# Performance work log

Measured on AMD Instinct MI355X. Metric: run time of the kernel, lower is better.

## Reference

```python
import jax, jax.numpy as jnp
import numpy as np

HIDDEN = 768
NUM_HEADS = 12
HEAD_DIM = HIDDEN // NUM_HEADS
QMAX = 127.0
DOMAIN_MIN, DOMAIN_MAX = -10.0, 0.0
NUM_INTERVALS = 12


def _build_pla_coeffs():
    # Least-squares linear fit of exp(x) on each of 12 uniform intervals of [-10, 0].
    xs = np.linspace(DOMAIN_MIN, DOMAIN_MAX, 1001)
    ys = np.exp(xs)
    edges = np.linspace(DOMAIN_MIN, DOMAIN_MAX, NUM_INTERVALS + 1)
    ms, cs = [], []
    for i in range(NUM_INTERVALS):
        mask = (xs >= edges[i]) & (xs <= edges[i + 1])
        m, c = np.polyfit(xs[mask], ys[mask], 1)
        ms.append(m)
        cs.append(c)
    # 'intervals' buffer holds the left endpoints a_i (length 12), as in torch code
    return (np.asarray(ms, np.float32), np.asarray(cs, np.float32),
            edges[:NUM_INTERVALS].astype(np.float32))

_PLA_M, _PLA_C, _PLA_A = _build_pla_coeffs()


def pla_exp(x):
    m = jnp.asarray(_PLA_M)
    c = jnp.asarray(_PLA_C)
    a = jnp.asarray(_PLA_A)
    xc = jnp.clip(x, DOMAIN_MIN, DOMAIN_MAX)
    # sum(xc >= a_i) - 1 == searchsorted(a, xc, side='right') - 1 (a is sorted)
    idx = jnp.clip(jnp.searchsorted(a, xc, side='right') - 1, 0, NUM_INTERVALS - 2)
    return m[idx] * xc + c[idx]


def pla_softmax(scores):
    shifted = scores - jnp.max(scores, axis=-1, keepdims=True)
    exps = pla_exp(shifted)
    return exps / (jnp.sum(exps, axis=-1, keepdims=True) + 1e-9)


def quant_linear(x, w_int8, w_scale, bias):
    # Dynamic per-token symmetric int8 quantization of activations.
    abs_max = jnp.max(jnp.abs(x), axis=-1, keepdims=True)
    input_scale = abs_max / QMAX
    input_scale = jnp.where(input_scale == 0.0, 1.0, input_scale)
    x_q = jnp.clip(jnp.round(x / input_scale), -128.0, 127.0)  # int8 values in fp32
    out = x_q @ w_int8.astype(jnp.float32).T                   # simulated int32 accum
    out = out * w_scale * input_scale                          # dequant rescale
    return out + bias


def setup_inputs() -> dict:
    key = jax.random.key(0)
    ks = jax.random.split(key, 16)
    B, S = 4, 1024
    inp = {
        'hidden_states': jax.random.normal(ks[0], (B, S, HIDDEN), jnp.float32),
        'attention_mask': jnp.zeros((B, 1, 1, S), jnp.float32),
    }
    for i, name in enumerate(['q', 'k', 'v', 'o']):
        kw, ksc, kb = ks[1 + 3 * i], ks[2 + 3 * i], ks[3 + 3 * i]
        inp[f'w{name}_int8'] = jax.random.randint(kw, (HIDDEN, HIDDEN), 0, 256, jnp.int32) - 128
        inp[f'w{name}_scale'] = jax.random.uniform(ksc, (HIDDEN,), jnp.float32) * 1e-4
        inp[f'b{name}'] = jax.random.normal(kb, (HIDDEN,), jnp.float32)
    return inp


def reference(hidden_states, attention_mask,
              wq_int8, wq_scale, bq,
              wk_int8, wk_scale, bk,
              wv_int8, wv_scale, bv,
              wo_int8, wo_scale, bo):
    B, S, H = hidden_states.shape
    scale = HEAD_DIM ** -0.5

    def split_heads(x):  # [B,S,H] -> [B,nh,S,hd]
        return x.reshape(B, S, NUM_HEADS, HEAD_DIM).transpose(0, 2, 1, 3)

    q = split_heads(quant_linear(hidden_states, wq_int8, wq_scale, bq))
    k = split_heads(quant_linear(hidden_states, wk_int8, wk_scale, bk))
    v = split_heads(quant_linear(hidden_states, wv_int8, wv_scale, bv))

    attn_scores = jnp.einsum('bhqd,bhkd->bhqk', q, k) * scale
    attn_scores = attn_scores + attention_mask
    attn_probs = pla_softmax(attn_scores)  # dropout is identity in eval mode

    context = jnp.einsum('bhqk,bhkd->bhqd', attn_probs, v)
    context = context.transpose(0, 2, 1, 3).reshape(B, S, H)
    return quant_linear(context, wo_int8, wo_scale, bo)
```

## Files before the change

kernel.cpp:

```cpp
#include <hip/hip_runtime.h>
#include <stdint.h>
#include <cmath>

#define TOKENS 4096
#define HIDDEN 768
#define NHEADS 12
#define SEQ    1024
#define NBH    48

typedef int   int32x4 __attribute__((ext_vector_type(4)));
typedef float f32x4   __attribute__((ext_vector_type(4)));
typedef short short8  __attribute__((ext_vector_type(8)));

struct PlaCoeffs { float m[12]; float c[12]; };

#define WBYTES   ((size_t)HIDDEN * HIDDEN)
#define OFF_WQ    ((size_t)256)
#define OFF_WK    (OFF_WQ + WBYTES)
#define OFF_WV    (OFF_WK + WBYTES)
#define OFF_WO    (OFF_WV + WBYTES)
#define OFF_XQ1   (OFF_WO + WBYTES)
#define OFF_SC1   (OFF_XQ1 + (size_t)TOKENS * HIDDEN)
#define OFF_QH    (OFF_SC1 + (size_t)TOKENS * 4)
#define HB        ((size_t)NBH * SEQ * 64 * 2)
#define OFF_KH    (OFF_QH + HB)
#define OFF_VT    (OFF_KH + HB)
#define OFF_CTX   (OFF_VT + HB)
#define OFF_XQ2   (OFF_CTX + (size_t)TOKENS * HIDDEN * 4)
#define OFF_SC2   (OFF_XQ2 + (size_t)TOKENS * HIDDEN)

__device__ __forceinline__ unsigned short f2bf(float f) {
  unsigned int u = __float_as_uint(f);
  u = (u + 0x7fffu + ((u >> 16) & 1u)) >> 16;
  return (unsigned short)u;
}

__device__ __forceinline__ unsigned int cvtpk_bf16(float a, float b) {
  unsigned int r;
  asm volatile("v_cvt_pk_bf16_f32 %0, %1, %2" : "=v"(r) : "v"(a), "v"(b));
  return r;
}

static PlaCoeffs compute_pla_coeffs() {
  PlaCoeffs out;
  const double step_e = 10.0 / 12.0;
  for (int i = 0; i < 12; i++) {
    double e0 = (double)i * step_e + (-10.0);
    double e1 = (i + 1 == 12) ? 0.0 : (double)(i + 1) * step_e + (-10.0);
    double n = 0.0, Sx = 0.0, Sy = 0.0, Sxy = 0.0, Sxx = 0.0;
    for (int j = 0; j <= 1000; j++) {
      double x = (j == 1000) ? 0.0 : (double)j * 0.01 + (-10.0);
      if (x >= e0 && x <= e1) {
        double y = std::exp(x);
        n += 1.0; Sx += x; Sy += y; Sxy += x * y; Sxx += x * x;
      }
    }
    double det = n * Sxx - Sx * Sx;
    double m = (n * Sxy - Sx * Sy) / det;
    double c = (Sy - m * Sx) / n;
    out.m[i] = (float)m;
    out.c[i] = (float)c;
  }
  return out;
}
static const PlaCoeffs g_pla = compute_pla_coeffs();

__global__ void prep_kernel(const float* __restrict__ x, signed char* __restrict__ xq,
                            float* __restrict__ sc,
                            const int* __restrict__ w0, const int* __restrict__ w1,
                            const int* __restrict__ w2, const int* __restrict__ w3,
                            signed char* __restrict__ o0, signed char* __restrict__ o1,
                            signed char* __restrict__ o2, signed char* __restrict__ o3) {
  int tid = threadIdx.x;
  if (blockIdx.x < TOKENS) {
    int t = blockIdx.x;
    const float* row = x + (size_t)t * HIDDEN;
    float v0 = row[tid], v1 = row[tid + 256], v2 = row[tid + 512];
    float am = fmaxf(fabsf(v0), fmaxf(fabsf(v1), fabsf(v2)));
#pragma unroll
    for (int m = 1; m < 64; m <<= 1) am = fmaxf(am, __shfl_xor(am, m, 64));
    __shared__ float red[4];
    if ((tid & 63) == 0) red[tid >> 6] = am;
    __syncthreads();
    float total = fmaxf(fmaxf(red[0], red[1]), fmaxf(red[2], red[3]));
    float s = total / 127.0f;
    if (s == 0.0f) s = 1.0f;
    float q0 = fminf(fmaxf(rintf(v0 / s), -128.0f), 127.0f);
    float q1 = fminf(fmaxf(rintf(v1 / s), -128.0f), 127.0f);
    float q2 = fminf(fmaxf(rintf(v2 / s), -128.0f), 127.0f);
    signed char* orow = xq + (size_t)t * HIDDEN;
    orow[tid]       = (signed char)(int)q0;
    orow[tid + 256] = (signed char)(int)q1;
    orow[tid + 512] = (signed char)(int)q2;
    if (tid == 0) sc[t] = s;
  } else {
    int p = blockIdx.x - TOKENS;
    int z = p / 576, px = p % 576;
    const int* src = z == 0 ? w0 : z == 1 ? w1 : z == 2 ? w2 : w3;
    signed char* dst = z == 0 ? o0 : z == 1 ? o1 : z == 2 ? o2 : o3;
    int idx = (px * 256 + tid) * 4;
    int32x4 v = *(const int32x4*)(src + idx);
    int packed = (v[0] & 255) | ((v[1] & 255) << 8) | ((v[2] & 255) << 16) | (v[3] << 24);
    *(int*)(dst + idx) = packed;
  }
}

__global__ void quant_kernel(const float* __restrict__ x, signed char* __restrict__ xq,
                             float* __restrict__ sc) {
  int t = blockIdx.x;
  int tid = threadIdx.x;
  const float* row = x + (size_t)t * HIDDEN;
  float v0 = row[tid], v1 = row[tid + 256], v2 = row[tid + 512];
  float am = fmaxf(fabsf(v0), fmaxf(fabsf(v1), fabsf(v2)));
#pragma unroll
  for (int m = 1; m < 64; m <<= 1) am = fmaxf(am, __shfl_xor(am, m, 64));
  __shared__ float red[4];
  if ((tid & 63) == 0) red[tid >> 6] = am;
  __syncthreads();
  float total = fmaxf(fmaxf(red[0], red[1]), fmaxf(red[2], red[3]));
  float s = total / 127.0f;
  if (s == 0.0f) s = 1.0f;
  float q0 = fminf(fmaxf(rintf(v0 / s), -128.0f), 127.0f);
  float q1 = fminf(fmaxf(rintf(v1 / s), -128.0f), 127.0f);
  float q2 = fminf(fmaxf(rintf(v2 / s), -128.0f), 127.0f);
  signed char* orow = xq + (size_t)t * HIDDEN;
  orow[tid]       = (signed char)(int)q0;
  orow[tid + 256] = (signed char)(int)q1;
  orow[tid + 512] = (signed char)(int)q2;
  if (tid == 0) sc[t] = s;
}

__device__ __forceinline__ void i8_mainloop(const signed char* __restrict__ Abase,
                                            const signed char* __restrict__ Bbase,
                                            char* As, char* Bs, int tid,
                                            int32x4 acc[4][4]) {
  int lane = tid & 63, w = tid >> 6;
  int lr = lane & 15, lg = lane >> 4;
  int wr = w >> 1, wc = w & 1;
  int laneoff = (lane >> 3) * HIDDEN + (((lane & 7) ^ (lane >> 3)) * 16);
  int rowblk = w * 32;

#pragma unroll
  for (int ii = 0; ii < 4; ii++) {
    const signed char* sa = Abase + (size_t)(rowblk + ii * 8) * HIDDEN + laneoff;
    const signed char* sb = Bbase + (size_t)(rowblk + ii * 8) * HIDDEN + laneoff;
    __builtin_amdgcn_global_load_lds(
        (const __attribute__((address_space(1))) void*)sa,
        (__attribute__((address_space(3))) void*)(As + (w * 4 + ii) * 1024), 16, 0, 0);
    __builtin_amdgcn_global_load_lds(
        (const __attribute__((address_space(1))) void*)sb,
        (__attribute__((address_space(3))) void*)(Bs + (w * 4 + ii) * 1024), 16, 0, 0);
  }
  __syncthreads();

  int buf = 0;
  for (int ks = 0; ks < 6; ks++) {
    if (ks < 5) {
      char* An = As + (buf ^ 1) * 16384;
      char* Bn = Bs + (buf ^ 1) * 16384;
#pragma unroll
      for (int ii = 0; ii < 4; ii++) {
        const signed char* sa =
            Abase + (size_t)(rowblk + ii * 8) * HIDDEN + (ks + 1) * 128 + laneoff;
        const signed char* sb =
            Bbase + (size_t)(rowblk + ii * 8) * HIDDEN + (ks + 1) * 128 + laneoff;
        __builtin_amdgcn_global_load_lds(
            (const __attribute__((address_space(1))) void*)sa,
            (__attribute__((address_space(3))) void*)(An + (w * 4 + ii) * 1024), 16, 0, 0);
        __builtin_amdgcn_global_load_lds(
            (const __attribute__((address_space(1))) void*)sb,
            (__attribute__((address_space(3))) void*)(Bn + (w * 4 + ii) * 1024), 16, 0, 0);
      }
    }
    const char* Ac = As + buf * 16384;
    const char* Bc = Bs + buf * 16384;
#pragma unroll
    for (int ksub = 0; ksub < 2; ksub++) {
      int32x4 af[4], bf[4];
      int cs = (ksub * 4 + lg) ^ (lr & 7);
#pragma unroll
      for (int i = 0; i < 4; i++)
        af[i] = *(const int32x4*)(Ac + (wr * 64 + i * 16 + lr) * 128 + cs * 16);
#pragma unroll
      for (int j = 0; j < 4; j++)
        bf[j] = *(const int32x4*)(Bc + (wc * 64 + j * 16 + lr) * 128 + cs * 16);
#pragma unroll
      for (int i = 0; i < 4; i++)
#pragma unroll
        for (int j = 0; j < 4; j++)
          acc[i][j] = __builtin_amdgcn_mfma_i32_16x16x64_i8(af[i], bf[j], acc[i][j], 0, 0, 0);
    }
    __syncthreads();
    buf ^= 1;
  }
}

__launch_bounds__(256, 2)
__global__ void qkv_gemm(const signed char* __restrict__ xq, const float* __restrict__ isc,
                         const signed char* __restrict__ wq, const signed char* __restrict__ wk,
                         const signed char* __restrict__ wv,
                         const float* __restrict__ wsq, const float* __restrict__ wsk,
                         const float* __restrict__ wsv,
                         const float* __restrict__ bq, const float* __restrict__ bk,
                         const float* __restrict__ bv,
                         unsigned short* __restrict__ qh, unsigned short* __restrict__ kh,
                         unsigned short* __restrict__ vt) {
  __shared__ __align__(16) char As[2 * 16384];
  __shared__ __align__(16) char Bs[2 * 16384];
  int z = blockIdx.z;
  const signed char* w   = z == 0 ? wq  : z == 1 ? wk  : wv;
  const float*       wsc = z == 0 ? wsq : z == 1 ? wsk : wsv;
  const float*       bias= z == 0 ? bq  : z == 1 ? bk  : bv;
  unsigned short*    out = z == 0 ? qh  : z == 1 ? kh  : vt;

  int tid = threadIdx.x;
  int lane = tid & 63, wave = tid >> 6;
  int lr = lane & 15, lg = lane >> 4;
  int mbase0 = blockIdx.x * 128;
  int mbase = mbase0 + (wave >> 1) * 64;
  int nbase = blockIdx.y * 128 + (wave & 1) * 64;

  int32x4 acc[4][4];
#pragma unroll
  for (int i = 0; i < 4; i++)
#pragma unroll
    for (int j = 0; j < 4; j++) acc[i][j] = (int32x4){0, 0, 0, 0};

  i8_mainloop(xq + (size_t)mbase0 * HIDDEN,
              w + (size_t)blockIdx.y * 128 * HIDDEN, As, Bs, tid, acc);

  if (z < 2) {
#pragma unroll
    for (int j = 0; j < 4; j++) {
      int col = nbase + j * 16 + lr;
      float wsv_ = wsc[col], bv_ = bias[col];
      int h = col >> 6, d = col & 63;
#pragma unroll
      for (int i = 0; i < 4; i++) {
#pragma unroll
        for (int r = 0; r < 4; r++) {
          int trow = mbase + i * 16 + lg * 4 + r;
          float v = (float)acc[i][j][r] * wsv_ * isc[trow] + bv_;
          int bb = trow >> 10, ss = trow & 1023;
          out[(((size_t)(bb * NHEADS + h)) * SEQ + ss) * 64 + d] = f2bf(v);
        }
      }
    }
  } else {
    unsigned short* T = (unsigned short*)As;
#pragma unroll
    for (int j = 0; j < 4; j++) {
      int colc = (wave & 1) * 64 + j * 16 + lr;
      int gcol = blockIdx.y * 128 + colc;
      float wsv_ = wsc[gcol], bv_ = bias[gcol];
      int rlb = (wave >> 1) * 64 + lg * 4;
#pragma unroll
      for (int i = 0; i < 4; i++) {
        int rl = rlb + i * 16;
        float v0 = (float)acc[i][j][0] * wsv_ * isc[mbase0 + rl + 0] + bv_;
        float v1 = (float)acc[i][j][1] * wsv_ * isc[mbase0 + rl + 1] + bv_;
        float v2 = (float)acc[i][j][2] * wsv_ * isc[mbase0 + rl + 2] + bv_;
        float v3 = (float)acc[i][j][3] * wsv_ * isc[mbase0 + rl + 3] + bv_;
        int oct = (rl >> 3) ^ (colc & 7);
        unsigned short* dst = T + colc * 128 + (oct << 3) + (rl & 7);
        *(unsigned int*)(dst)     = cvtpk_bf16(v0, v1);
        *(unsigned int*)(dst + 2) = cvtpk_bf16(v2, v3);
      }
    }
    __syncthreads();
    int bb = mbase0 >> 10, ssb = mbase0 & 1023;
    int o = tid & 15, cb = (tid >> 4) * 8;
#pragma unroll
    for (int j = 0; j < 8; j++) {
      int colc = cb + j;
      int gcol = blockIdx.y * 128 + colc;
      int hh = gcol >> 6, dd = gcol & 63;
      unsigned short* g = out + (((size_t)(bb * NHEADS + hh)) * 64 + dd) * SEQ + ssb + o * 8;
      *(short8*)g = *(const short8*)(T + colc * 128 + ((o ^ (colc & 7)) << 3));
    }
  }
}

__launch_bounds__(256, 2)
__global__ void o_gemm(const signed char* __restrict__ xq, const float* __restrict__ isc,
                       const signed char* __restrict__ w, const float* __restrict__ wsc,
                       const float* __restrict__ bias, float* __restrict__ out) {
  __shared__ __align__(16) char As[2 * 16384];
  __shared__ __align__(16) char Bs[2 * 16384];
  int tid = threadIdx.x;
  int lane = tid & 63, wave = tid >> 6;
  int lr = lane & 15, lg = lane >> 4;
  int mbase = blockIdx.x * 128 + (wave >> 1) * 64;
  int nbase = blockIdx.y * 128 + (wave & 1) * 64;

  int32x4 acc[4][4];
#pragma unroll
  for (int i = 0; i < 4; i++)
#pragma unroll
    for (int j = 0; j < 4; j++) acc[i][j] = (int32x4){0, 0, 0, 0};

  i8_mainloop(xq + (size_t)blockIdx.x * 128 * HIDDEN,
              w + (size_t)blockIdx.y * 128 * HIDDEN, As, Bs, tid, acc);

#pragma unroll
  for (int j = 0; j < 4; j++) {
    int col = nbase + j * 16 + lr;
    float wsv_ = wsc[col], bv_ = bias[col];
#pragma unroll
    for (int i = 0; i < 4; i++) {
#pragma unroll
      for (int r = 0; r < 4; r++) {
        int trow = mbase + i * 16 + lg * 4 + r;
        float v = (float)acc[i][j][r] * wsv_ * isc[trow] + bv_;
        out[(size_t)trow * HIDDEN + col] = v;
      }
    }
  }
}

__launch_bounds__(512, 6)
__global__ void attn_kernel(const unsigned short* __restrict__ qh,
                            const unsigned short* __restrict__ kgl,
                            const unsigned short* __restrict__ vt,
                            const float* __restrict__ mask,
                            const PlaCoeffs cf,
                            float* __restrict__ ctx) {
  __shared__ __align__(16) char smem[49152];
  unsigned short* kbuf = (unsigned short*)smem;
  unsigned short* vbuf = (unsigned short*)(smem + 16384);
  unsigned short* plds = (unsigned short*)(smem + 32768);
  float* parts = (float*)smem;
  __shared__ float rmaxp[8][16], rmaxv[4][16], rsump[8][16], rsumv[4][16];
  __shared__ float2 lmc[12];

  int tid = threadIdx.x;
  int lane = tid & 63, w = tid >> 6;
  int lr = lane & 15, lg = lane >> 4;
  int m = w & 3, kh2 = w >> 2;

  if (tid < 12) lmc[tid] = make_float2(cf.m[tid], cf.c[tid]);

  int nb = (blockIdx.x & 7) * 96 + (blockIdx.x >> 3);
  int bh = nb >> 4, qt = nb & 15;
  int b = bh / NHEADS, h = bh % NHEADS;
  int qbase = qt * 64;

  const unsigned short* qp     = qh + ((size_t)bh * SEQ + qbase + m * 16) * 64;
  const unsigned short* khead  = kgl + (size_t)bh * SEQ * 64;
  const unsigned short* vthead = vt + (size_t)bh * 64 * SEQ;
  const float* mrow = mask + b * SEQ;

  short8 qa0 = *(const short8*)(qp + (size_t)lr * 64 + lg * 8);
  short8 qa1 = *(const short8*)(qp + (size_t)lr * 64 + 32 + lg * 8);

  int sr = tid >> 3, sd = (tid & 7) * 8;
  int sidx = sr * 64 + (sd ^ ((sr & 7) << 3));
  const unsigned short* kgp = khead + (size_t)sr * 64 + sd;
  const unsigned short* vgp = vthead + (size_t)sr * 1024 + sd;

  float rm[4] = {-3.0e38f, -3.0e38f, -3.0e38f, -3.0e38f};
  short8 stk = *(const short8*)kgp;
  for (int c = 0; c < 16; c++) {
    unsigned short* kb = kbuf + (c & 1) * 4096;
    *(short8*)(kb + sidx) = stk;
    if (c < 15) stk = *(const short8*)(kgp + (size_t)(c + 1) * 4096);
    __syncthreads();
#pragma unroll
    for (int kt = 0; kt < 2; kt++) {
      int krow = kh2 * 32 + kt * 16 + lr;
      const unsigned short* kbp = kb + krow * 64;
      int sw = (krow & 7) << 3;
      short8 k0 = *(const short8*)(kbp + ((lg * 8) ^ sw));
      short8 k1 = *(const short8*)(kbp + ((32 + lg * 8) ^ sw));
      f32x4 a = {0.f, 0.f, 0.f, 0.f};
      __builtin_amdgcn_s_setprio(1);
      a = __builtin_amdgcn_mfma_f32_16x16x32_bf16(qa0, k0, a, 0, 0, 0);
      a = __builtin_amdgcn_mfma_f32_16x16x32_bf16(qa1, k1, a, 0, 0, 0);
      __builtin_amdgcn_s_setprio(0);
      float mk = mrow[c * 64 + krow];
#pragma unroll
      for (int r = 0; r < 4; r++) rm[r] = fmaxf(rm[r], fmaf(a[r], 0.125f, mk));
    }
  }
#pragma unroll
  for (int r = 0; r < 4; r++) {
#pragma unroll
    for (int msk = 1; msk < 16; msk <<= 1) rm[r] = fmaxf(rm[r], __shfl_xor(rm[r], msk, 64));
  }
  if (lr == 0) {
#pragma unroll
    for (int r = 0; r < 4; r++) rmaxp[w][lg * 4 + r] = rm[r];
  }
  __syncthreads();
  if (tid < 64) {
    int mm = tid >> 4, row = tid & 15;
    rmaxv[mm][row] = fmaxf(rmaxp[mm][row], rmaxp[mm + 4][row]);
  }
  __syncthreads();

  float rmx[4], rs[4];
#pragma unroll
  for (int r = 0; r < 4; r++) { rmx[r] = rmaxv[m][lg * 4 + r]; rs[r] = 0.f; }
  f32x4 pacc[4];
#pragma unroll
  for (int n = 0; n < 4; n++) pacc[n] = (f32x4){0.f, 0.f, 0.f, 0.f};
  unsigned short* pw = plds + w * 1024;

  short8 stk2 = *(const short8*)kgp;
  short8 stv  = *(const short8*)vgp;
  for (int c = 0; c < 16; c++) {
    unsigned short* kb = kbuf + (c & 1) * 4096;
    unsigned short* vb = vbuf + (c & 1) * 4096;
    *(short8*)(kb + sidx) = stk2;
    *(short8*)(vb + sidx) = stv;
    if (c < 15) {
      stk2 = *(const short8*)(kgp + (size_t)(c + 1) * 4096);
      stv  = *(const short8*)(vgp + (c + 1) * 64);
    }
    __syncthreads();
#pragma unroll
    for (int kt = 0; kt < 2; kt++) {
      int krow = kh2 * 32 + kt * 16 + lr;
      const unsigned short* kbp = kb + krow * 64;
      int sw = (krow & 7) << 3;
      short8 k0 = *(const short8*)(kbp + ((lg * 8) ^ sw));
      short8 k1 = *(const short8*)(kbp + ((32 + lg * 8) ^ sw));
      f32x4 a = {0.f, 0.f, 0.f, 0.f};
      __builtin_amdgcn_s_setprio(1);
      a = __builtin_amdgcn_mfma_f32_16x16x32_bf16(qa0, k0, a, 0, 0, 0);
      a = __builtin_amdgcn_mfma_f32_16x16x32_bf16(qa1, k1, a, 0, 0, 0);
      __builtin_amdgcn_s_setprio(0);
      float mk = mrow[c * 64 + krow];
      float p[4];
#pragma unroll
      for (int r = 0; r < 4; r++) {
        float x = fmaf(a[r], 0.125f, mk) - rmx[r];
        x = fminf(fmaxf(x, -10.f), 0.f);
        int ii = (int)fmaf(x, 1.2f, 12.0f);
        ii = ii > 10 ? 10 : ii;
        float2 mc = lmc[ii];
        p[r] = fmaf(mc.x, x, mc.y);
        rs[r] += p[r];
      }
      unsigned int pk01 = cvtpk_bf16(p[0], p[1]);
      unsigned int pk23 = cvtpk_bf16(p[2], p[3]);
      int colw = kt * 16 + lr;
      int r0 = lg * 4;
      pw[(r0 + 0) * 64 + (colw ^ (((r0 + 0) & 7) << 3))] = (unsigned short)pk01;
      pw[(r0 + 1) * 64 + (colw ^ (((r0 + 1) & 7) << 3))] = (unsigned short)(pk01 >> 16);
      pw[(r0 + 2) * 64 + (colw ^ (((r0 + 2) & 7) << 3))] = (unsigned short)pk23;
      pw[(r0 + 3) * 64 + (colw ^ (((r0 + 3) & 7) << 3))] = (unsigned short)(pk23 >> 16);
    }
    short8 pa = *(const short8*)(pw + lr * 64 + ((lg * 8) ^ ((lr & 7) << 3)));
    __builtin_amdgcn_s_setprio(1);
#pragma unroll
    for (int n = 0; n < 4; n++) {
      int d = n * 16 + lr;
      short8 vv = *(const short8*)(vb + d * 64 + ((kh2 * 32 + lg * 8) ^ ((d & 7) << 3)));
      pacc[n] = __builtin_amdgcn_mfma_f32_16x16x32_bf16(pa, vv, pacc[n], 0, 0, 0);
    }
    __builtin_amdgcn_s_setprio(0);
  }

#pragma unroll
  for (int r = 0; r < 4; r++) {
#pragma unroll
    for (int msk = 1; msk < 16; msk <<= 1) rs[r] += __shfl_xor(rs[r], msk, 64);
  }
  if (lr == 0) {
#pragma unroll
    for (int r = 0; r < 4; r++) rsump[w][lg * 4 + r] = rs[r];
  }
  __syncthreads();
  {
    float* pslice = parts + w * 1024;
#pragma unroll
    for (int n = 0; n < 4; n++)
#pragma unroll
      for (int r = 0; r < 4; r++)
        pslice[(lg * 4 + r) * 64 + n * 16 + lr] = pacc[n][r];
  }
  if (tid < 64) {
    int mm = tid >> 4, row = tid & 15;
    rsumv[mm][row] = rsump[mm][row] + rsump[mm + 4][row];
  }
  __syncthreads();

  {
    int mm = tid >> 7, row = (tid >> 3) & 15, c8 = (tid & 7) * 8;
    float dn = rsumv[mm][row] + 1e-9f;
    const float* p0 = parts + (mm * 16 + row) * 64 + c8;
    const float* p1 = p0 + 4 * 1024;
    f32x4 a0 = *(const f32x4*)p0, a1 = *(const f32x4*)(p0 + 4);
    f32x4 b0 = *(const f32x4*)p1, b1 = *(const f32x4*)(p1 + 4);
    f32x4 o0 = {(a0[0] + b0[0]) / dn, (a0[1] + b0[1]) / dn,
                (a0[2] + b0[2]) / dn, (a0[3] + b0[3]) / dn};
    f32x4 o1 = {(a1[0] + b1[0]) / dn, (a1[1] + b1[1]) / dn,
                (a1[2] + b1[2]) / dn, (a1[3] + b1[3]) / dn};
    float* op = &ctx[((size_t)b * SEQ + qbase + mm * 16 + row) * HIDDEN + h * 64 + c8];
    *(f32x4*)op = o0;
    *(f32x4*)(op + 4) = o1;
  }
}

extern "C" void kernel_launch(void* const* d_in, const int* in_sizes, int n_in,
                              void* d_out, int out_size, void* d_ws, size_t ws_size,
                              hipStream_t stream) {
  const float* hidden = (const float*)d_in[0];
  const float* mask   = (const float*)d_in[1];
  const int*   wq  = (const int*)d_in[2];
  const float* wsq = (const float*)d_in[3];
  const float* bq  = (const float*)d_in[4];
  const int*   wk  = (const int*)d_in[5];
  const float* wsk = (const float*)d_in[6];
  const float* bk  = (const float*)d_in[7];
  const int*   wv  = (const int*)d_in[8];
  const float* wsv = (const float*)d_in[9];
  const float* bv  = (const float*)d_in[10];
  const int*   wo  = (const int*)d_in[11];
  const float* wso = (const float*)d_in[12];
  const float* bo  = (const float*)d_in[13];

  char* ws = (char*)d_ws;
  signed char*    pwq   = (signed char*)(ws + OFF_WQ);
  signed char*    pwk   = (signed char*)(ws + OFF_WK);
  signed char*    pwv   = (signed char*)(ws + OFF_WV);
  signed char*    pwo   = (signed char*)(ws + OFF_WO);
  signed char*    xq1   = (signed char*)(ws + OFF_XQ1);
  float*          sc1   = (float*)(ws + OFF_SC1);
  unsigned short* qhp   = (unsigned short*)(ws + OFF_QH);
  unsigned short* khp   = (unsigned short*)(ws + OFF_KH);
  unsigned short* vtp   = (unsigned short*)(ws + OFF_VT);
  float*          ctxp  = (float*)(ws + OFF_CTX);
  signed char*    xq2   = (signed char*)(ws + OFF_XQ2);
  float*          sc2   = (float*)(ws + OFF_SC2);

  prep_kernel<<<TOKENS + 2304, 256, 0, stream>>>(hidden, xq1, sc1,
                                                 wq, wk, wv, wo, pwq, pwk, pwv, pwo);
  qkv_gemm<<<dim3(32, 6, 3), 256, 0, stream>>>(xq1, sc1, pwq, pwk, pwv,
                                               wsq, wsk, wsv, bq, bk, bv,
                                               qhp, khp, vtp);
  attn_kernel<<<768, 512, 0, stream>>>(qhp, khp, vtp, mask, g_pla, ctxp);
  quant_kernel<<<TOKENS, 256, 0, stream>>>(ctxp, xq2, sc2);
  o_gemm<<<dim3(32, 6, 1), 256, 0, stream>>>(xq2, sc2, pwo, wso, bo, (float*)d_out);
}
```

Baseline: 93.19 us.

## Cache attention scores in registers and split keys four ways per block

The attention kernel now handles 32 query rows per block with four waves splitting the key dimension, doubling the grid to 1536 blocks. Scores from the first pass are kept in registers (16 f32x4 per thread), so the second pass loads only V and no longer recomputes QK^T or reloads K. The K/V tiles grow to 128 keys with new swizzles, and partial outputs are reduced across four waves. The cost is much higher register pressure (launch bounds lowered to 4 blocks), more redundant K/V loads per query row, and a heavier cross-wave reduction.

After: 109.4 us. 1.17x slower.

```diff
diff --git a/kernel.cpp b/kernel.cpp
--- a/kernel.cpp
+++ b/kernel.cpp
@@ -318,32 +318,29 @@
   }
 }
 
-__launch_bounds__(512, 6)
+__launch_bounds__(512, 4)
 __global__ void attn_kernel(const unsigned short* __restrict__ qh,
                             const unsigned short* __restrict__ kgl,
                             const unsigned short* __restrict__ vt,
                             const float* __restrict__ mask,
                             const PlaCoeffs cf,
                             float* __restrict__ ctx) {
-  __shared__ __align__(16) char smem[49152];
-  unsigned short* kbuf = (unsigned short*)smem;
-  unsigned short* vbuf = (unsigned short*)(smem + 16384);
-  unsigned short* plds = (unsigned short*)(smem + 32768);
-  float* parts = (float*)smem;
-  __shared__ float rmaxp[8][16], rmaxv[4][16], rsump[8][16], rsumv[4][16];
+  __shared__ __align__(16) char smem[32768];
+  __shared__ __align__(16) unsigned short plds[8][512];
+  __shared__ float rmaxp[8][16], rmaxv[2][16], rsump[8][16], rsumv[2][16];
   __shared__ float2 lmc[12];
 
   int tid = threadIdx.x;
   int lane = tid & 63, w = tid >> 6;
   int lr = lane & 15, lg = lane >> 4;
-  int m = w & 3, kh2 = w >> 2;
+  int m = w >> 2, ks = w & 3;
 
   if (tid < 12) lmc[tid] = make_float2(cf.m[tid], cf.c[tid]);
 
-  int nb = (blockIdx.x & 7) * 96 + (blockIdx.x >> 3);
-  int bh = nb >> 4, qt = nb & 15;
+  int nb = (blockIdx.x & 7) * 192 + (blockIdx.x >> 3);
+  int bh = nb >> 5, qt = nb & 31;
   int b = bh / NHEADS, h = bh % NHEADS;
-  int qbase = qt * 64;
+  int qbase = qt * 32;
 
   const unsigned short* qp     = qh + ((size_t)bh * SEQ + qbase + m * 16) * 64;
   const unsigned short* khead  = kgl + (size_t)bh * SEQ * 64;
@@ -353,35 +350,48 @@
   short8 qa0 = *(const short8*)(qp + (size_t)lr * 64 + lg * 8);
   short8 qa1 = *(const short8*)(qp + (size_t)lr * 64 + 32 + lg * 8);
 
-  int sr = tid >> 3, sd = (tid & 7) * 8;
-  int sidx = sr * 64 + (sd ^ ((sr & 7) << 3));
-  const unsigned short* kgp = khead + (size_t)sr * 64 + sd;
-  const unsigned short* vgp = vthead + (size_t)sr * 1024 + sd;
-
+  int s_ = tid >> 2, dk = (tid & 3) * 16;
+  int ksw = (s_ & 7) << 4;
+  int kofs0 = s_ * 128 + ((dk * 2) ^ ksw);
+  int kofs1 = s_ * 128 + ((dk * 2 + 16) ^ ksw);
+  const unsigned short* kgA = khead + (size_t)s_ * 64 + dk;
+
+  f32x4 sc[16];
   float rm[4] = {-3.0e38f, -3.0e38f, -3.0e38f, -3.0e38f};
-  short8 stk = *(const short8*)kgp;
-  for (int c = 0; c < 16; c++) {
-    unsigned short* kb = kbuf + (c & 1) * 4096;
-    *(short8*)(kb + sidx) = stk;
-    if (c < 15) stk = *(const short8*)(kgp + (size_t)(c + 1) * 4096);
+  short8 stka = *(const short8*)kgA;
+  short8 stkb = *(const short8*)(kgA + 8);
+#pragma unroll
+  for (int c = 0; c < 8; c++) {
+    char* dst = smem + (c & 1) * 16384;
+    *(short8*)(dst + kofs0) = stka;
+    *(short8*)(dst + kofs1) = stkb;
+    if (c < 7) {
+      stka = *(const short8*)(kgA + (size_t)(c + 1) * 8192);
+      stkb = *(const short8*)(kgA + (size_t)(c + 1) * 8192 + 8);
+    }
     __syncthreads();
+    const char* kb = smem + (c & 1) * 16384;
 #pragma unroll
     for (int kt = 0; kt < 2; kt++) {
-      int krow = kh2 * 32 + kt * 16 + lr;
-      const unsigned short* kbp = kb + krow * 64;
-      int sw = (krow & 7) << 3;
-      short8 k0 = *(const short8*)(kbp + ((lg * 8) ^ sw));
-      short8 k1 = *(const short8*)(kbp + ((32 + lg * 8) ^ sw));
+      int krow = ks * 32 + kt * 16 + lr;
+      int sw = (krow & 7) << 4;
+      short8 k0 = *(const short8*)(kb + krow * 128 + ((lg * 16) ^ sw));
+      short8 k1 = *(const short8*)(kb + krow * 128 + ((64 + lg * 16) ^ sw));
       f32x4 a = {0.f, 0.f, 0.f, 0.f};
       __builtin_amdgcn_s_setprio(1);
       a = __builtin_amdgcn_mfma_f32_16x16x32_bf16(qa0, k0, a, 0, 0, 0);
       a = __builtin_amdgcn_mfma_f32_16x16x32_bf16(qa1, k1, a, 0, 0, 0);
       __builtin_amdgcn_s_setprio(0);
-      float mk = mrow[c * 64 + krow];
-#pragma unroll
-      for (int r = 0; r < 4; r++) rm[r] = fmaxf(rm[r], fmaf(a[r], 0.125f, mk));
-    }
-  }
+      float mk = mrow[c * 128 + krow];
+#pragma unroll
+      for (int r = 0; r < 4; r++) {
+        float x = fmaf(a[r], 0.125f, mk);
+        sc[c * 2 + kt][r] = x;
+        rm[r] = fmaxf(rm[r], x);
+      }
+    }
+  }
+
 #pragma unroll
   for (int r = 0; r < 4; r++) {
 #pragma unroll
@@ -392,9 +402,12 @@
     for (int r = 0; r < 4; r++) rmaxp[w][lg * 4 + r] = rm[r];
   }
   __syncthreads();
-  if (tid < 64) {
+  if (tid < 32) {
     int mm = tid >> 4, row = tid & 15;
-    rmaxv[mm][row] = fmaxf(rmaxp[mm][row], rmaxp[mm + 4][row]);
+    float mv = rmaxp[mm * 4][row];
+#pragma unroll
+    for (int c = 1; c < 4; c++) mv = fmaxf(mv, rmaxp[mm * 4 + c][row]);
+    rmaxv[mm][row] = mv;
   }
   __syncthreads();
 
@@ -404,37 +417,32 @@
   f32x4 pacc[4];
 #pragma unroll
   for (int n = 0; n < 4; n++) pacc[n] = (f32x4){0.f, 0.f, 0.f, 0.f};
-  unsigned short* pw = plds + w * 1024;
-
-  short8 stk2 = *(const short8*)kgp;
-  short8 stv  = *(const short8*)vgp;
-  for (int c = 0; c < 16; c++) {
-    unsigned short* kb = kbuf + (c & 1) * 4096;
-    unsigned short* vb = vbuf + (c & 1) * 4096;
-    *(short8*)(kb + sidx) = stk2;
-    *(short8*)(vb + sidx) = stv;
-    if (c < 15) {
-      stk2 = *(const short8*)(kgp + (size_t)(c + 1) * 4096);
-      stv  = *(const short8*)(vgp + (c + 1) * 64);
+  unsigned short* pw = plds[w];
+
+  int vd = tid >> 3, vs = (tid & 7) * 16;
+  int vsw = (vd & 7) << 4;
+  int vofs0 = vd * 256 + ((vs * 2) ^ vsw);
+  int vofs1 = vd * 256 + ((vs * 2 + 16) ^ vsw);
+  const unsigned short* vgA = vthead + (size_t)vd * SEQ + vs;
+
+  short8 stva = *(const short8*)vgA;
+  short8 stvb = *(const short8*)(vgA + 8);
+#pragma unroll
+  for (int cp = 0; cp < 8; cp++) {
+    char* dst = smem + (cp & 1) * 16384;
+    *(short8*)(dst + vofs0) = stva;
+    *(short8*)(dst + vofs1) = stvb;
+    if (cp < 7) {
+      stva = *(const short8*)(vgA + (cp + 1) * 128);
+      stvb = *(const short8*)(vgA + (cp + 1) * 128 + 8);
     }
     __syncthreads();
 #pragma unroll
     for (int kt = 0; kt < 2; kt++) {
-      int krow = kh2 * 32 + kt * 16 + lr;
-      const unsigned short* kbp = kb + krow * 64;
-      int sw = (krow & 7) << 3;
-      short8 k0 = *(const short8*)(kbp + ((lg * 8) ^ sw));
-      short8 k1 = *(const short8*)(kbp + ((32 + lg * 8) ^ sw));
-      f32x4 a = {0.f, 0.f, 0.f, 0.f};
-      __builtin_amdgcn_s_setprio(1);
-      a = __builtin_amdgcn_mfma_f32_16x16x32_bf16(qa0, k0, a, 0, 0, 0);
-      a = __builtin_amdgcn_mfma_f32_16x16x32_bf16(qa1, k1, a, 0, 0, 0);
-      __builtin_amdgcn_s_setprio(0);
-      float mk = mrow[c * 64 + krow];
       float p[4];
 #pragma unroll
       for (int r = 0; r < 4; r++) {
-        float x = fmaf(a[r], 0.125f, mk) - rmx[r];
+        float x = sc[cp * 2 + kt][r] - rmx[r];
         x = fminf(fmaxf(x, -10.f), 0.f);
         int ii = (int)fmaf(x, 1.2f, 12.0f);
         ii = ii > 10 ? 10 : ii;
@@ -446,17 +454,18 @@
       unsigned int pk23 = cvtpk_bf16(p[2], p[3]);
       int colw = kt * 16 + lr;
       int r0 = lg * 4;
-      pw[(r0 + 0) * 64 + (colw ^ (((r0 + 0) & 7) << 3))] = (unsigned short)pk01;
-      pw[(r0 + 1) * 64 + (colw ^ (((r0 + 1) & 7) << 3))] = (unsigned short)(pk01 >> 16);
-      pw[(r0 + 2) * 64 + (colw ^ (((r0 + 2) & 7) << 3))] = (unsigned short)pk23;
-      pw[(r0 + 3) * 64 + (colw ^ (((r0 + 3) & 7) << 3))] = (unsigned short)(pk23 >> 16);
-    }
-    short8 pa = *(const short8*)(pw + lr * 64 + ((lg * 8) ^ ((lr & 7) << 3)));
+      pw[(r0 + 0) * 32 + (colw ^ 0)]           = (unsigned short)pk01;
+      pw[(r0 + 1) * 32 + (colw ^ 8)]           = (unsigned short)(pk01 >> 16);
+      pw[(r0 + 2) * 32 + (colw ^ 16)]          = (unsigned short)pk23;
+      pw[(r0 + 3) * 32 + (colw ^ 24)]          = (unsigned short)(pk23 >> 16);
+    }
+    short8 pa = *(const short8*)((const char*)pw + lr * 64 + (((lg * 8) ^ ((lr & 3) << 3)) * 2));
+    const char* vb = smem + (cp & 1) * 16384;
     __builtin_amdgcn_s_setprio(1);
 #pragma unroll
     for (int n = 0; n < 4; n++) {
       int d = n * 16 + lr;
-      short8 vv = *(const short8*)(vb + d * 64 + ((kh2 * 32 + lg * 8) ^ ((d & 7) << 3)));
+      short8 vv = *(const short8*)(vb + d * 256 + ((ks * 64 + lg * 16) ^ ((d & 7) << 4)));
       pacc[n] = __builtin_amdgcn_mfma_f32_16x16x32_bf16(pa, vv, pacc[n], 0, 0, 0);
     }
     __builtin_amdgcn_s_setprio(0);
@@ -473,33 +482,37 @@
   }
   __syncthreads();
   {
-    float* pslice = parts + w * 1024;
+    float* ps = (float*)smem + w * 1024;
 #pragma unroll
     for (int n = 0; n < 4; n++)
 #pragma unroll
-      for (int r = 0; r < 4; r++)
-        pslice[(lg * 4 + r) * 64 + n * 16 + lr] = pacc[n][r];
-  }
-  if (tid < 64) {
+      for (int r = 0; r < 4; r++) {
+        int row = lg * 4 + r;
+        ps[row * 64 + ((n * 16 + lr) ^ ((row & 7) << 2))] = pacc[n][r];
+      }
+  }
+  if (tid < 32) {
     int mm = tid >> 4, row = tid & 15;
-    rsumv[mm][row] = rsump[mm][row] + rsump[mm + 4][row];
+    float sv = rsump[mm * 4][row];
+#pragma unroll
+    for (int c = 1; c < 4; c++) sv += rsump[mm * 4 + c][row];
+    rsumv[mm][row] = sv;
   }
   __syncthreads();
 
   {
-    int mm = tid >> 7, row = (tid >> 3) & 15, c8 = (tid & 7) * 8;
-    float dn = rsumv[mm][row] + 1e-9f;
-    const float* p0 = parts + (mm * 16 + row) * 64 + c8;
-    const float* p1 = p0 + 4 * 1024;
-    f32x4 a0 = *(const f32x4*)p0, a1 = *(const f32x4*)(p0 + 4);
-    f32x4 b0 = *(const f32x4*)p1, b1 = *(const f32x4*)(p1 + 4);
-    f32x4 o0 = {(a0[0] + b0[0]) / dn, (a0[1] + b0[1]) / dn,
-                (a0[2] + b0[2]) / dn, (a0[3] + b0[3]) / dn};
-    f32x4 o1 = {(a1[0] + b1[0]) / dn, (a1[1] + b1[1]) / dn,
-                (a1[2] + b1[2]) / dn, (a1[3] + b1[3]) / dn};
-    float* op = &ctx[((size_t)b * SEQ + qbase + mm * 16 + row) * HIDDEN + h * 64 + c8];
-    *(f32x4*)op = o0;
-    *(f32x4*)(op + 4) = o1;
+    int m2 = tid >> 8, row = (tid >> 4) & 15, c4 = (tid & 15) * 4;
+    float dn = rsumv[m2][row] + 1e-9f;
+    int co = (c4 ^ ((row & 7) << 2)) + row * 64;
+    const float* base = (const float*)smem + m2 * 4 * 1024;
+    f32x4 a0 = *(const f32x4*)(base + co);
+    f32x4 a1 = *(const f32x4*)(base + 1024 + co);
+    f32x4 a2 = *(const f32x4*)(base + 2048 + co);
+    f32x4 a3 = *(const f32x4*)(base + 3072 + co);
+    f32x4 o;
+#pragma unroll
+    for (int j = 0; j < 4; j++) o[j] = (a0[j] + a1[j] + a2[j] + a3[j]) / dn;
+    *(f32x4*)&ctx[((size_t)b * SEQ + qbase + m2 * 16 + row) * HIDDEN + h * 64 + c4] = o;
   }
 }
 
@@ -540,7 +553,7 @@
   qkv_gemm<<<dim3(32, 6, 3), 256, 0, stream>>>(xq1, sc1, pwq, pwk, pwv,
                                                wsq, wsk, wsv, bq, bk, bv,
                                                qhp, khp, vtp);
-  attn_kernel<<<768, 512, 0, stream>>>(qhp, khp, vtp, mask, g_pla, ctxp);
+  attn_kernel<<<1536, 512, 0, stream>>>(qhp, khp, vtp, mask, g_pla, ctxp);
   quant_kernel<<<TOKENS, 256, 0, stream>>>(ctxp, xq2, sc2);
   o_gemm<<<dim3(32, 6, 1), 256, 0, stream>>>(xq2, sc2, pwo, wso, bo, (float*)d_out);
 }
```

## Shrink attention LDS footprint by aliasing reductions and shuffling PLA coefficients

Applied to the files above, without the earlier changes.

Cuts the attention kernel's shared memory from 48 KB plus side arrays to 40 KB. The row max/sum scratch arrays now alias the K/V buffers. The per-wave P staging tile shrinks to 16x32 with a new swizzle. The PLA coefficient table moves from LDS into lane registers and is read with cross-lane shuffles. The goal is more resident blocks per CU under the launch bounds, at the cost of extra barriers, two shuffles per element in the hot loop, and a risk of aliasing bugs.

After: 103.4 us. 1.11x slower.

```diff
diff --git a/kernel.cpp b/kernel.cpp
--- a/kernel.cpp
+++ b/kernel.cpp
@@ -325,20 +325,23 @@
                             const float* __restrict__ mask,
                             const PlaCoeffs cf,
                             float* __restrict__ ctx) {
-  __shared__ __align__(16) char smem[49152];
+  __shared__ __align__(16) char smem[40960];
   unsigned short* kbuf = (unsigned short*)smem;
   unsigned short* vbuf = (unsigned short*)(smem + 16384);
   unsigned short* plds = (unsigned short*)(smem + 32768);
   float* parts = (float*)smem;
-  __shared__ float rmaxp[8][16], rmaxv[4][16], rsump[8][16], rsumv[4][16];
-  __shared__ float2 lmc[12];
+  float* rmaxp = (float*)(smem + 16384);
+  float* rmaxv = (float*)(smem + 16384 + 512);
+  float* rsump = (float*)(smem + 32768);
+  float* rsumv = (float*)(smem + 32768 + 512);
 
   int tid = threadIdx.x;
   int lane = tid & 63, w = tid >> 6;
   int lr = lane & 15, lg = lane >> 4;
   int m = w & 3, kh2 = w >> 2;
 
-  if (tid < 12) lmc[tid] = make_float2(cf.m[tid], cf.c[tid]);
+  float pm = 0.f, pc = 0.f;
+  if (lane < 12) { pm = cf.m[lane]; pc = cf.c[lane]; }
 
   int nb = (blockIdx.x & 7) * 96 + (blockIdx.x >> 3);
   int bh = nb >> 4, qt = nb & 15;
@@ -389,22 +392,24 @@
   }
   if (lr == 0) {
 #pragma unroll
-    for (int r = 0; r < 4; r++) rmaxp[w][lg * 4 + r] = rm[r];
+    for (int r = 0; r < 4; r++) rmaxp[w * 16 + lg * 4 + r] = rm[r];
   }
   __syncthreads();
   if (tid < 64) {
     int mm = tid >> 4, row = tid & 15;
-    rmaxv[mm][row] = fmaxf(rmaxp[mm][row], rmaxp[mm + 4][row]);
+    rmaxv[mm * 16 + row] = fmaxf(rmaxp[mm * 16 + row], rmaxp[(mm + 4) * 16 + row]);
   }
   __syncthreads();
 
   float rmx[4], rs[4];
 #pragma unroll
-  for (int r = 0; r < 4; r++) { rmx[r] = rmaxv[m][lg * 4 + r]; rs[r] = 0.f; }
+  for (int r = 0; r < 4; r++) { rmx[r] = rmaxv[m * 16 + lg * 4 + r]; rs[r] = 0.f; }
+  __syncthreads();
+
   f32x4 pacc[4];
 #pragma unroll
   for (int n = 0; n < 4; n++) pacc[n] = (f32x4){0.f, 0.f, 0.f, 0.f};
-  unsigned short* pw = plds + w * 1024;
+  unsigned short* pw = plds + w * 512;
 
   short8 stk2 = *(const short8*)kgp;
   short8 stv  = *(const short8*)vgp;
@@ -438,20 +443,22 @@
         x = fminf(fmaxf(x, -10.f), 0.f);
         int ii = (int)fmaf(x, 1.2f, 12.0f);
         ii = ii > 10 ? 10 : ii;
-        float2 mc = lmc[ii];
-        p[r] = fmaf(mc.x, x, mc.y);
+        float mcx = __shfl(pm, ii, 64);
+        float mcy = __shfl(pc, ii, 64);
+        p[r] = fmaf(mcx, x, mcy);
         rs[r] += p[r];
       }
       unsigned int pk01 = cvtpk_bf16(p[0], p[1]);
       unsigned int pk23 = cvtpk_bf16(p[2], p[3]);
       int colw = kt * 16 + lr;
-      int r0 = lg * 4;
-      pw[(r0 + 0) * 64 + (colw ^ (((r0 + 0) & 7) << 3))] = (unsigned short)pk01;
-      pw[(r0 + 1) * 64 + (colw ^ (((r0 + 1) & 7) << 3))] = (unsigned short)(pk01 >> 16);
-      pw[(r0 + 2) * 64 + (colw ^ (((r0 + 2) & 7) << 3))] = (unsigned short)pk23;
-      pw[(r0 + 3) * 64 + (colw ^ (((r0 + 3) & 7) << 3))] = (unsigned short)(pk23 >> 16);
-    }
-    short8 pa = *(const short8*)(pw + lr * 64 + ((lg * 8) ^ ((lr & 7) << 3)));
+      int lgb = (lg & 1) << 4;
+      pw[(lg * 4 + 0) * 32 + (colw ^ 0  ^ lgb)] = (unsigned short)pk01;
+      pw[(lg * 4 + 1) * 32 + (colw ^ 8  ^ lgb)] = (unsigned short)(pk01 >> 16);
+      pw[(lg * 4 + 2) * 32 + (colw ^ 16 ^ lgb)] = (unsigned short)pk23;
+      pw[(lg * 4 + 3) * 32 + (colw ^ 24 ^ lgb)] = (unsigned short)(pk23 >> 16);
+    }
+    short8 pa = *(const short8*)(pw + lr * 32 +
+                                 ((lg * 8) ^ ((lr & 3) << 3) ^ (((lr >> 2) & 1) << 4)));
     __builtin_amdgcn_s_setprio(1);
 #pragma unroll
     for (int n = 0; n < 4; n++) {
@@ -467,11 +474,11 @@
 #pragma unroll
     for (int msk = 1; msk < 16; msk <<= 1) rs[r] += __shfl_xor(rs[r], msk, 64);
   }
+  __syncthreads();
   if (lr == 0) {
 #pragma unroll
-    for (int r = 0; r < 4; r++) rsump[w][lg * 4 + r] = rs[r];
-  }
-  __syncthreads();
+    for (int r = 0; r < 4; r++) rsump[w * 16 + lg * 4 + r] = rs[r];
+  }
   {
     float* pslice = parts + w * 1024;
 #pragma unroll
@@ -480,15 +487,16 @@
       for (int r = 0; r < 4; r++)
         pslice[(lg * 4 + r) * 64 + n * 16 + lr] = pacc[n][r];
   }
+  __syncthreads();
   if (tid < 64) {
     int mm = tid >> 4, row = tid & 15;
-    rsumv[mm][row] = rsump[mm][row] + rsump[mm + 4][row];
+    rsumv[mm * 16 + row] = rsump[mm * 16 + row] + rsump[(mm + 4) * 16 + row];
   }
   __syncthreads();
 
   {
     int mm = tid >> 7, row = (tid >> 3) & 15, c8 = (tid & 7) * 8;
-    float dn = rsumv[mm][row] + 1e-9f;
+    float dn = rsumv[mm * 16 + row] + 1e-9f;
     const float* p0 = parts + (mm * 16 + row) * 64 + c8;
     const float* p1 = p0 + 4 * 1024;
     f32x4 a0 = *(const f32x4*)p0, a1 = *(const f32x4*)(p0 + 4);
```

## Software-pipeline PV MFMA one chunk behind QK in attention loop

Applied to the files above, without the earlier changes.

Restructures the attention inner loop so the P·V MFMAs for the previous key chunk are issued right after the current chunk's QK MFMAs. The P tile is double-buffered in LDS, and V fragments are held in registers across iterations. This is meant to overlap the softmax VALU work with matrix-core work and hide LDS latency. In exchange it doubles the per-wave P staging (LDS grows to 64KB) and lowers the launch-bounds occupancy hint from 6 to 4, which means fewer resident blocks and more register pressure.

After: 96.90 us. 1.04x slower.

```diff
diff --git a/kernel.cpp b/kernel.cpp
--- a/kernel.cpp
+++ b/kernel.cpp
@@ -318,14 +318,14 @@
   }
 }
 
-__launch_bounds__(512, 6)
+__launch_bounds__(512, 4)
 __global__ void attn_kernel(const unsigned short* __restrict__ qh,
                             const unsigned short* __restrict__ kgl,
                             const unsigned short* __restrict__ vt,
                             const float* __restrict__ mask,
                             const PlaCoeffs cf,
                             float* __restrict__ ctx) {
-  __shared__ __align__(16) char smem[49152];
+  __shared__ __align__(16) char smem[65536];
   unsigned short* kbuf = (unsigned short*)smem;
   unsigned short* vbuf = (unsigned short*)(smem + 16384);
   unsigned short* plds = (unsigned short*)(smem + 32768);
@@ -404,11 +404,14 @@
   f32x4 pacc[4];
 #pragma unroll
   for (int n = 0; n < 4; n++) pacc[n] = (f32x4){0.f, 0.f, 0.f, 0.f};
-  unsigned short* pw = plds + w * 1024;
+  unsigned short* pw = plds + w * 2048;
+  int paoff = lr * 64 + ((lg * 8) ^ ((lr & 7) << 3));
 
   short8 stk2 = *(const short8*)kgp;
   short8 stv  = *(const short8*)vgp;
-  for (int c = 0; c < 16; c++) {
+  short8 vvA[4], vvB[4];
+
+  auto chunk = [&](int c, short8* vprev, short8* vcur) {
     unsigned short* kb = kbuf + (c & 1) * 4096;
     unsigned short* vb = vbuf + (c & 1) * 4096;
     *(short8*)(kb + sidx) = stk2;
@@ -418,6 +421,14 @@
       stv  = *(const short8*)(vgp + (c + 1) * 64);
     }
     __syncthreads();
+#pragma unroll
+    for (int n = 0; n < 4; n++) {
+      int d = n * 16 + lr;
+      vcur[n] = *(const short8*)(vb + d * 64 + ((kh2 * 32 + lg * 8) ^ ((d & 7) << 3)));
+    }
+    short8 pa;
+    if (c > 0) pa = *(const short8*)(pw + ((c - 1) & 1) * 1024 + paoff);
+    unsigned short* pw2 = pw + (c & 1) * 1024;
 #pragma unroll
     for (int kt = 0; kt < 2; kt++) {
       int krow = kh2 * 32 + kt * 16 + lr;
@@ -429,6 +440,11 @@
       __builtin_amdgcn_s_setprio(1);
       a = __builtin_amdgcn_mfma_f32_16x16x32_bf16(qa0, k0, a, 0, 0, 0);
       a = __builtin_amdgcn_mfma_f32_16x16x32_bf16(qa1, k1, a, 0, 0, 0);
+      if (kt == 0 && c > 0) {
+#pragma unroll
+        for (int n = 0; n < 4; n++)
+          pacc[n] = __builtin_amdgcn_mfma_f32_16x16x32_bf16(pa, vprev[n], pacc[n], 0, 0, 0);
+      }
       __builtin_amdgcn_s_setprio(0);
       float mk = mrow[c * 64 + krow];
       float p[4];
@@ -446,19 +462,23 @@
       unsigned int pk23 = cvtpk_bf16(p[2], p[3]);
       int colw = kt * 16 + lr;
       int r0 = lg * 4;
-      pw[(r0 + 0) * 64 + (colw ^ (((r0 + 0) & 7) << 3))] = (unsigned short)pk01;
-      pw[(r0 + 1) * 64 + (colw ^ (((r0 + 1) & 7) << 3))] = (unsigned short)(pk01 >> 16);
-      pw[(r0 + 2) * 64 + (colw ^ (((r0 + 2) & 7) << 3))] = (unsigned short)pk23;
-      pw[(r0 + 3) * 64 + (colw ^ (((r0 + 3) & 7) << 3))] = (unsigned short)(pk23 >> 16);
-    }
-    short8 pa = *(const short8*)(pw + lr * 64 + ((lg * 8) ^ ((lr & 7) << 3)));
+      pw2[(r0 + 0) * 64 + (colw ^ (((r0 + 0) & 7) << 3))] = (unsigned short)pk01;
+      pw2[(r0 + 1) * 64 + (colw ^ (((r0 + 1) & 7) << 3))] = (unsigned short)(pk01 >> 16);
+      pw2[(r0 + 2) * 64 + (colw ^ (((r0 + 2) & 7) << 3))] = (unsigned short)pk23;
+      pw2[(r0 + 3) * 64 + (colw ^ (((r0 + 3) & 7) << 3))] = (unsigned short)(pk23 >> 16);
+    }
+  };
+
+  for (int cc = 0; cc < 16; cc += 2) {
+    chunk(cc, vvB, vvA);
+    chunk(cc + 1, vvA, vvB);
+  }
+  {
+    short8 pa = *(const short8*)(pw + 1024 + paoff);
     __builtin_amdgcn_s_setprio(1);
 #pragma unroll
-    for (int n = 0; n < 4; n++) {
-      int d = n * 16 + lr;
-      short8 vv = *(const short8*)(vb + d * 64 + ((kh2 * 32 + lg * 8) ^ ((d & 7) << 3)));
-      pacc[n] = __builtin_amdgcn_mfma_f32_16x16x32_bf16(pa, vv, pacc[n], 0, 0, 0);
-    }
+    for (int n = 0; n < 4; n++)
+      pacc[n] = __builtin_amdgcn_mfma_f32_16x16x32_bf16(pa, vvB[n], pacc[n], 0, 0, 0);
     __builtin_amdgcn_s_setprio(0);
   }
 
```
